# Kernel optimization log

Hardware: AMD Instinct MI355X
Metric: run time of the kernel (lower is better)

The kernel has to match this reference:

```python
import jax, jax.numpy as jnp
import numpy as np

N, D, R, O = 4096, 128, 256, 64


def setup_inputs() -> dict:
    key = jax.random.key(0)
    k1, k2, k3, k4 = jax.random.split(key, 4)
    X = jax.random.normal(k1, (N, D), dtype=jnp.float32)
    # Gaussian membership params per rule: centers and (positive) widths, shape [R, D]
    centers = 0.5 * jax.random.normal(k2, (R, D), dtype=jnp.float32)
    sigmas = 1.5 + jax.random.uniform(k3, (R, D), dtype=jnp.float32)  # in [1.5, 2.5]
    # Takagi-Sugeno per-rule linear coeffs [R, D+1, O] (last row = bias)
    coeffs = 0.02 * jax.random.normal(k4, (R, D + 1, O), dtype=jnp.float32)
    return {"X": X, "centers": centers, "sigmas": sigmas, "coeffs": coeffs}


def reference(X, centers, sigmas, coeffs):
    # Layer 1: Gaussian memberships for all rules at once: [N, R, D]
    diff = X[:, None, :] - centers[None, :, :]
    memb = jnp.exp(-(diff * diff) / (2.0 * sigmas * sigmas)[None, :, :])
    # Layer 2: rule strengths via product over input dims ('prod' strategy): [N, R]
    strengths = jnp.prod(memb, axis=2)
    # Layer 3: normalize across rules
    norm = strengths / (jnp.sum(strengths, axis=1, keepdims=True) + 1e-8)
    # Layer 4: per-rule linear consequents: [N, R, O]
    weighted = jnp.einsum('ni,rij->nrj', X, coeffs[:, :-1, :]) + coeffs[:, -1, :][None, :, :]
    # Layer 5: weighted combine over rules: [N, O]
    out = jnp.einsum('nr,nrj->nj', norm, weighted)
    # task='classification' -> Softmax(dim=1)
    return jax.nn.softmax(out, axis=1)
```

## Files before the change

kernel.cpp:

```cpp
#include <hip/hip_runtime.h>

#define N_SAMPLES 4096
#define D_IN      128
#define R_RULES   256
#define O_OUT     64
#define KPAD      136
#define NCHUNK    17
#define CH_I      8
#define NGROUPS   8

typedef _Float16 f16;
typedef _Float16 f16x2 __attribute__((ext_vector_type(2)));
typedef _Float16 f16x4 __attribute__((ext_vector_type(4)));
typedef _Float16 f16x8 __attribute__((ext_vector_type(8)));
typedef float    f32x4 __attribute__((ext_vector_type(4)));

__global__ __launch_bounds__(256) void anfis_prep_all(
    const float* __restrict__ coeffs, const float* __restrict__ centers,
    const float* __restrict__ sigmas, f16* __restrict__ Cp,
    f16* __restrict__ Bext) {
  __shared__ alignas(16) f16 T[64 * 32];
  __shared__ float red[4];
  const int bid = blockIdx.x;
  const int tid = threadIdx.x;

  if (bid < 1088) {
    const int g = bid / 136;
    const int i = bid - g * 136;
    const int rg = tid & 31;
    const int jb = tid >> 5;
    if (i < 129) {
      const float* src = coeffs + ((size_t)(g * 32 + rg) * 129 + i) * 64 + jb * 8;
      float4 a = reinterpret_cast<const float4*>(src)[0];
      float4 b = reinterpret_cast<const float4*>(src)[1];
      T[(jb * 8 + 0) * 32 + rg] = (f16)a.x;
      T[(jb * 8 + 1) * 32 + rg] = (f16)a.y;
      T[(jb * 8 + 2) * 32 + rg] = (f16)a.z;
      T[(jb * 8 + 3) * 32 + rg] = (f16)a.w;
      T[(jb * 8 + 4) * 32 + rg] = (f16)b.x;
      T[(jb * 8 + 5) * 32 + rg] = (f16)b.y;
      T[(jb * 8 + 6) * 32 + rg] = (f16)b.z;
      T[(jb * 8 + 7) * 32 + rg] = (f16)b.w;
    } else {
#pragma unroll
      for (int q = 0; q < 8; ++q) T[(jb * 8 + q) * 32 + rg] = (f16)0.0f;
    }
    __syncthreads();
    f16x8* dst = reinterpret_cast<f16x8*>(Cp + ((size_t)g * KPAD + i) * 2048);
    const int j = tid >> 2, blk = tid & 3;
    dst[(j << 2) | blk] = reinterpret_cast<const f16x8*>(T)[tid];
  } else {
    const int sub = tid >> 7;
    const int d = tid & 127;
    const int r = ((bid - 1088) << 1) + sub;
    const float c = centers[(size_t)r * 128 + d];
    const float s = sigmas[(size_t)r * 128 + d];
    const float iv = 0.5f / (s * s);
    const float b1 = -iv;
    const float b2 = 2.0f * c * iv;
    f16 b1h = (f16)b1; f16 b1l = (f16)(b1 - (float)b1h);
    f16 b2h = (f16)b2; f16 b2l = (f16)(b2 - (float)b2h);
    auto put = [&](int k, f16 v) {
      Bext[((size_t)(k >> 3) * 256 + r) * 8 + (k & 7)] = v;
    };
    put(d, b1h);
    put(128 + d, b1l);
    put(256 + d, b1h);
    put(384 + d, b2h);
    put(512 + d, b2l);
    put(640 + d, b2h);
    float p = -c * c * iv;
#pragma unroll
    for (int off = 32; off; off >>= 1) p += __shfl_xor(p, off, 64);
    if ((tid & 63) == 0) red[tid >> 6] = p;
    __syncthreads();
    if (d < 30) put(770 + d, (f16)0.0f);
    if (d == 0) {
      float k2 = red[sub * 2] + red[sub * 2 + 1];
      f16 h = (f16)k2; f16 l = (f16)(k2 - (float)h);
      put(768, h);
      put(769, l);
    }
  }
}

__global__ __launch_bounds__(512) void anfis_s16n(
    const float* __restrict__ X, const f16* __restrict__ Bext,
    f16* __restrict__ P) {
  __shared__ alignas(16) f16 Xq[16 * 512];
  __shared__ float rowsum[16][8];
  const int tid = threadIdx.x;
  const int m0 = blockIdx.x * 16;
  const int w = tid >> 6, lane = tid & 63;
  const int lm = lane & 15, quad = lane >> 4;

  if (tid < 256) {
    int m = tid >> 4, oct = tid & 15;
    const float* src = X + (size_t)(m0 + m) * 128 + oct * 8;
    float4 a = reinterpret_cast<const float4*>(src)[0];
    float4 b = reinterpret_cast<const float4*>(src)[1];
    float xs[8] = {a.x, a.y, a.z, a.w, b.x, b.y, b.z, b.w};
    f16x8 vh, vl, v2h, v2l;
#pragma unroll
    for (int q = 0; q < 8; ++q) {
      float x = xs[q];
      f16 h = (f16)x;   f16 l = (f16)(x - (float)h);
      float x2 = x * x;
      f16 h2 = (f16)x2; f16 l2 = (f16)(x2 - (float)h2);
      vh[q] = h; vl[q] = l; v2h[q] = h2; v2l[q] = l2;
    }
    f16x8* row = reinterpret_cast<f16x8*>(&Xq[m * 512]);
    int sw = m & 7;
    row[(0 * 16 + oct) ^ sw] = v2h;
    row[(1 * 16 + oct) ^ sw] = v2l;
    row[(2 * 16 + oct) ^ sw] = vh;
    row[(3 * 16 + oct) ^ sw] = vl;
  }
  __syncthreads();

  f32x4 acc[2] = {};
  const f16x8* arow = reinterpret_cast<const f16x8*>(&Xq[lm * 512]);
  const int asw = lm & 7;
  const int col0 = w * 32 + lm;

#pragma unroll
  for (int t = 0; t < 24; ++t) {
    const int seg = t >> 2;
    const int plane = (seg < 2) ? 0 : (seg == 2) ? 1 : (seg < 5) ? 2 : 3;
    const int o = t * 4 + quad;
    f16x8 av = arow[(plane * 16 + (o & 15)) ^ asw];
    const f16* bp = Bext + ((size_t)o * 256 + col0) * 8;
    f16x8 b0 = *reinterpret_cast<const f16x8*>(bp);
    f16x8 b1 = *reinterpret_cast<const f16x8*>(bp + 16 * 8);
    acc[0] = __builtin_amdgcn_mfma_f32_16x16x32_f16(av, b0, acc[0], 0, 0, 0);
    acc[1] = __builtin_amdgcn_mfma_f32_16x16x32_f16(av, b1, acc[1], 0, 0, 0);
  }
  {
    f16x8 av = {};
    if (quad == 0) { av[0] = (f16)1.0f; av[1] = (f16)1.0f; }
    const int o = 96 + quad;
    const f16* bp = Bext + ((size_t)o * 256 + col0) * 8;
    f16x8 b0 = *reinterpret_cast<const f16x8*>(bp);
    f16x8 b1 = *reinterpret_cast<const f16x8*>(bp + 16 * 8);
    acc[0] = __builtin_amdgcn_mfma_f32_16x16x32_f16(av, b0, acc[0], 0, 0, 0);
    acc[1] = __builtin_amdgcn_mfma_f32_16x16x32_f16(av, b1, acc[1], 0, 0, 0);
  }

  float e[2][4];
#pragma unroll
  for (int nf = 0; nf < 2; ++nf)
#pragma unroll
    for (int q = 0; q < 4; ++q) e[nf][q] = __expf(acc[nf][q]);

  float rp[4];
#pragma unroll
  for (int q = 0; q < 4; ++q) {
    rp[q] = e[0][q] + e[1][q];
#pragma unroll
    for (int msk = 1; msk < 16; msk <<= 1) rp[q] += __shfl_xor(rp[q], msk, 64);
  }
  if (lm == 0)
#pragma unroll
    for (int q = 0; q < 4; ++q) rowsum[quad * 4 + q][w] = rp[q];
  __syncthreads();

#pragma unroll
  for (int q = 0; q < 4; ++q) {
    const int row = quad * 4 + q;
    float s8 = 0.f;
#pragma unroll
    for (int w2 = 0; w2 < 8; ++w2) s8 += rowsum[row][w2];
    const float inv = 1.0f / (s8 + 1e-8f);
#pragma unroll
    for (int nf = 0; nf < 2; ++nf)
      P[(size_t)(m0 + row) * R_RULES + w * 32 + nf * 16 + lm] =
          (f16)(e[nf][q] * inv);
  }
}

__global__ __launch_bounds__(512) void anfis_main16(
    const float* __restrict__ X, const f16* __restrict__ P,
    const f16* __restrict__ Cp, float* __restrict__ part) {
  __shared__ alignas(16) f16 Xs[128 * KPAD];
  const int tid = threadIdx.x;
  const int g = blockIdx.x & 7;
  const int m0 = (blockIdx.x >> 3) * 128;
  const int w = tid >> 6, lane = tid & 63;
  const int mg = w >> 2;
  const int wc = w & 3;
  const int lm = lane & 15, quad = lane >> 4;

#pragma unroll
  for (int it = 0; it < 8; ++it) {
    int fi = tid + (it << 9);
    int m = fi >> 5, k4 = (fi & 31) << 2;
    float4 v = reinterpret_cast<const float4*>(X)[(size_t)(m0 + m) * 32 + (fi & 31)];
    f16x4 h = {(f16)v.x, (f16)v.y, (f16)v.z, (f16)v.w};
    *reinterpret_cast<f16x4*>(&Xs[m * KPAD + k4]) = h;
  }
  if (tid < 128) {
    f16x8 bias = {};
    bias[0] = (f16)1.0f;
    *reinterpret_cast<f16x8*>(&Xs[tid * KPAD + 128]) = bias;
  }

  union F8 { f16x8 v; f16x2 h[4]; };
  F8 pf[4];
#pragma unroll
  for (int mf = 0; mf < 4; ++mf) {
    int row = m0 + mg * 64 + mf * 16 + lm;
    pf[mf].v = *reinterpret_cast<const f16x8*>(
        &P[(size_t)row * R_RULES + g * 32 + quad * 8]);
  }

  __syncthreads();

  f32x4 acc[4] = {};
  const char* bsrc = (const char*)Cp + (size_t)g * KPAD * 4096 +
                     ((wc * 16 + lm) << 6) + (quad << 4);

  for (int c = 0; c < NCHUNK; ++c) {
    f16x8 xv[4];
#pragma unroll
    for (int mf = 0; mf < 4; ++mf)
      xv[mf] = *reinterpret_cast<const f16x8*>(
          &Xs[(mg * 64 + mf * 16 + lm) * KPAD + c * 8]);
#pragma unroll
    for (int ii = 0; ii < CH_I; ++ii) {
      f16x8 b0 = *reinterpret_cast<const f16x8*>(
          bsrc + (size_t)(c * 8 + ii) * 4096);
#pragma unroll
      for (int mf = 0; mf < 4; ++mf) {
        f16 xvv = xv[mf][ii];
        f16x2 xd = {xvv, xvv};
        F8 a;
        a.h[0] = pf[mf].h[0] * xd;
        a.h[1] = pf[mf].h[1] * xd;
        a.h[2] = pf[mf].h[2] * xd;
        a.h[3] = pf[mf].h[3] * xd;
        acc[mf] = __builtin_amdgcn_mfma_f32_16x16x32_f16(a.v, b0, acc[mf], 0, 0, 0);
      }
    }
  }

#pragma unroll
  for (int mf = 0; mf < 4; ++mf)
#pragma unroll
    for (int q = 0; q < 4; ++q) {
      int row = m0 + mg * 64 + mf * 16 + quad * 4 + q;
      int col = wc * 16 + lm;
      part[((size_t)g * N_SAMPLES + row) * O_OUT + col] = acc[mf][q];
    }
}

__global__ __launch_bounds__(256) void anfis_out(
    const float* __restrict__ part, float* __restrict__ out) {
  const int n = blockIdx.x * 4 + (threadIdx.x >> 6);
  const int lane = threadIdx.x & 63;
  const size_t stride = (size_t)N_SAMPLES * O_OUT;
  const float* p0 = part + (size_t)n * O_OUT + lane;
  float v = 0.f;
#pragma unroll
  for (int gg = 0; gg < 8; ++gg) v += p0[gg * stride];
  float mx = v;
#pragma unroll
  for (int off = 32; off; off >>= 1) mx = fmaxf(mx, __shfl_xor(mx, off, 64));
  float e = __expf(v - mx);
  float s = e;
#pragma unroll
  for (int off = 32; off; off >>= 1) s += __shfl_xor(s, off, 64);
  out[(size_t)n * O_OUT + lane] = e / s;
}

extern "C" void kernel_launch(void* const* d_in, const int* in_sizes, int n_in,
                              void* d_out, int out_size, void* d_ws, size_t ws_size,
                              hipStream_t stream) {
  const float* X       = (const float*)d_in[0];
  const float* centers = (const float*)d_in[1];
  const float* sigmas  = (const float*)d_in[2];
  const float* coeffs  = (const float*)d_in[3];
  float* out = (float*)d_out;

  float* part = (float*)d_ws;
  f16*   Cp   = (f16*)(part + (size_t)NGROUPS * N_SAMPLES * O_OUT);
  f16*   Bext = Cp + (size_t)NGROUPS * KPAD * 2048;
  f16*   P    = Bext + (size_t)100 * 256 * 8;

  anfis_prep_all<<<1088 + 128, 256, 0, stream>>>(coeffs, centers, sigmas, Cp, Bext);
  anfis_s16n<<<N_SAMPLES / 16, 512, 0, stream>>>(X, Bext, P);
  anfis_main16<<<256, 512, 0, stream>>>(X, P, Cp, part);
  anfis_out<<<N_SAMPLES / 4, 256, 0, stream>>>(part, out);
}
```

Baseline: 110.3 us.

## Rework consequent GEMM to 32x32 MFMA with LDS-staged double-buffered coefficients

The main consequent kernel now splits rules into 16 groups of 16 instead of 8 groups of 32 and uses 32x32x16 MFMA tiles. Coefficient tiles are streamed into shared memory with global_load_lds in a double-buffered loop, and X rows are read directly from global memory, replacing the shared-memory X staging. The prep kernel writes coefficients in a new layout to match, and the output kernel sums 16 partials instead of 8. The doubled partial buffer adds extra write and read traffic.

```diff
diff --git a/kernel.cpp b/kernel.cpp
--- a/kernel.cpp
+++ b/kernel.cpp
@@ -5,19 +5,19 @@
 #define R_RULES   256
 #define O_OUT     64
 #define KPAD      136
-#define NCHUNK    17
-#define CH_I      8
-#define NGROUPS   8
+#define NG16      16
+#define CP3_I     144
 
 typedef _Float16 f16;
 typedef _Float16 f16x2 __attribute__((ext_vector_type(2)));
 typedef _Float16 f16x4 __attribute__((ext_vector_type(4)));
 typedef _Float16 f16x8 __attribute__((ext_vector_type(8)));
 typedef float    f32x4 __attribute__((ext_vector_type(4)));
+typedef float    f32x16 __attribute__((ext_vector_type(16)));
 
 __global__ __launch_bounds__(256) void anfis_prep_all(
     const float* __restrict__ coeffs, const float* __restrict__ centers,
-    const float* __restrict__ sigmas, f16* __restrict__ Cp,
+    const float* __restrict__ sigmas, f16* __restrict__ Cp3,
     f16* __restrict__ Bext) {
   __shared__ alignas(16) f16 T[64 * 32];
   __shared__ float red[4];
@@ -25,12 +25,12 @@
   const int tid = threadIdx.x;
 
   if (bid < 1088) {
-    const int g = bid / 136;
-    const int i = bid - g * 136;
+    const int g8 = bid / 136;
+    const int i = bid - g8 * 136;
     const int rg = tid & 31;
     const int jb = tid >> 5;
     if (i < 129) {
-      const float* src = coeffs + ((size_t)(g * 32 + rg) * 129 + i) * 64 + jb * 8;
+      const float* src = coeffs + ((size_t)(g8 * 32 + rg) * 129 + i) * 64 + jb * 8;
       float4 a = reinterpret_cast<const float4*>(src)[0];
       float4 b = reinterpret_cast<const float4*>(src)[1];
       T[(jb * 8 + 0) * 32 + rg] = (f16)a.x;
@@ -46,9 +46,12 @@
       for (int q = 0; q < 8; ++q) T[(jb * 8 + q) * 32 + rg] = (f16)0.0f;
     }
     __syncthreads();
-    f16x8* dst = reinterpret_cast<f16x8*>(Cp + ((size_t)g * KPAD + i) * 2048);
-    const int j = tid >> 2, blk = tid & 3;
-    dst[(j << 2) | blk] = reinterpret_cast<const f16x8*>(T)[tid];
+    const int j = tid >> 2, oc = tid & 3;
+    const int g16 = g8 * 2 + (oc >> 1), rh = oc & 1;
+    const int jh = j >> 5, jl = j & 31;
+    f16x8* dst3 = reinterpret_cast<f16x8*>(Cp3);
+    dst3[(((size_t)g16 * CP3_I + i) * 2 + jh) * 64 + rh * 32 + jl] =
+        *reinterpret_cast<const f16x8*>(&T[j * 32 + oc * 8]);
   } else {
     const int sub = tid >> 7;
     const int d = tid & 127;
@@ -178,79 +181,104 @@
   }
 }
 
-__global__ __launch_bounds__(512) void anfis_main16(
+__global__ __launch_bounds__(512, 4) void anfis_rules32(
     const float* __restrict__ X, const f16* __restrict__ P,
-    const f16* __restrict__ Cp, float* __restrict__ part) {
-  __shared__ alignas(16) f16 Xs[128 * KPAD];
+    const f16* __restrict__ Cp3, float* __restrict__ part) {
+  __shared__ alignas(16) f16 Bs[2 * 16384];
   const int tid = threadIdx.x;
-  const int g = blockIdx.x & 7;
-  const int m0 = (blockIdx.x >> 3) * 128;
+  const int g = blockIdx.x & 15;
+  const int m0 = (blockIdx.x >> 4) * 128;
   const int w = tid >> 6, lane = tid & 63;
-  const int mg = w >> 2;
-  const int wc = w & 3;
-  const int lm = lane & 15, quad = lane >> 4;
-
-#pragma unroll
-  for (int it = 0; it < 8; ++it) {
-    int fi = tid + (it << 9);
-    int m = fi >> 5, k4 = (fi & 31) << 2;
-    float4 v = reinterpret_cast<const float4*>(X)[(size_t)(m0 + m) * 32 + (fi & 31)];
-    f16x4 h = {(f16)v.x, (f16)v.y, (f16)v.z, (f16)v.w};
-    *reinterpret_cast<f16x4*>(&Xs[m * KPAD + k4]) = h;
-  }
-  if (tid < 128) {
-    f16x8 bias = {};
-    bias[0] = (f16)1.0f;
-    *reinterpret_cast<f16x8*>(&Xs[tid * KPAD + 128]) = bias;
-  }
+  const int ms = w >> 1, jh = w & 1;
+  const int jl = lane & 31, rh = lane >> 5;
+  const int arow = m0 + ms * 32 + jl;
 
   union F8 { f16x8 v; f16x2 h[4]; };
-  F8 pf[4];
-#pragma unroll
-  for (int mf = 0; mf < 4; ++mf) {
-    int row = m0 + mg * 64 + mf * 16 + lm;
-    pf[mf].v = *reinterpret_cast<const f16x8*>(
-        &P[(size_t)row * R_RULES + g * 32 + quad * 8]);
-  }
-
+  F8 pf;
+  pf.v = *reinterpret_cast<const f16x8*>(&P[(size_t)arow * R_RULES + g * 16 + rh * 8]);
+
+  const float4* Xrow = reinterpret_cast<const float4*>(X + (size_t)arow * D_IN);
+  const char* cg = (const char*)Cp3 + (size_t)g * (CP3_I * 2048);
+  const int rdoff = jh * 512 + rh * 256 + jl * 8;
+
+  auto stage = [&](int buf, int ch) {
+    const char* gsrc = cg + (size_t)ch * 32768;
+#pragma unroll
+    for (int r = 0; r < 4; ++r) {
+      int off = (r << 13) + (w << 10);
+      __builtin_amdgcn_global_load_lds(
+          (const __attribute__((address_space(1))) unsigned int*)(gsrc + off + lane * 16),
+          (__attribute__((address_space(3))) unsigned int*)((char*)Bs + buf * 32768 + off),
+          16, 0, 0);
+    }
+  };
+
+  f16x8 xb[2][2];
+  auto cvt16 = [](float4 a, float4 b) {
+    f16x8 r = {(f16)a.x, (f16)a.y, (f16)a.z, (f16)a.w,
+               (f16)b.x, (f16)b.y, (f16)b.z, (f16)b.w};
+    return r;
+  };
+
+  stage(0, 0);
+  {
+    float4 f0 = Xrow[0], f1 = Xrow[1], f2 = Xrow[2], f3 = Xrow[3];
+    xb[0][0] = cvt16(f0, f1);
+    xb[0][1] = cvt16(f2, f3);
+  }
   __syncthreads();
 
-  f32x4 acc[4] = {};
-  const char* bsrc = (const char*)Cp + (size_t)g * KPAD * 4096 +
-                     ((wc * 16 + lm) << 6) + (quad << 4);
-
-  for (int c = 0; c < NCHUNK; ++c) {
-    f16x8 xv[4];
-#pragma unroll
-    for (int mf = 0; mf < 4; ++mf)
-      xv[mf] = *reinterpret_cast<const f16x8*>(
-          &Xs[(mg * 64 + mf * 16 + lm) * KPAD + c * 8]);
-#pragma unroll
-    for (int ii = 0; ii < CH_I; ++ii) {
-      f16x8 b0 = *reinterpret_cast<const f16x8*>(
-          bsrc + (size_t)(c * 8 + ii) * 4096);
-#pragma unroll
-      for (int mf = 0; mf < 4; ++mf) {
-        f16 xvv = xv[mf][ii];
-        f16x2 xd = {xvv, xvv};
-        F8 a;
-        a.h[0] = pf[mf].h[0] * xd;
-        a.h[1] = pf[mf].h[1] * xd;
-        a.h[2] = pf[mf].h[2] * xd;
-        a.h[3] = pf[mf].h[3] * xd;
-        acc[mf] = __builtin_amdgcn_mfma_f32_16x16x32_f16(a.v, b0, acc[mf], 0, 0, 0);
+  f32x16 acc = {};
+#pragma unroll
+  for (int ch = 0; ch < 8; ++ch) {
+    float4 f0, f1, f2, f3;
+    if (ch < 7) {
+      stage((ch + 1) & 1, ch + 1);
+      f0 = Xrow[(ch + 1) * 4 + 0];
+      f1 = Xrow[(ch + 1) * 4 + 1];
+      f2 = Xrow[(ch + 1) * 4 + 2];
+      f3 = Xrow[(ch + 1) * 4 + 3];
+    } else {
+      if (tid < 128) {
+        const char* gsrc = cg + (size_t)8 * 32768;
+        int off = (tid >> 6) << 10;
+        __builtin_amdgcn_global_load_lds(
+            (const __attribute__((address_space(1))) unsigned int*)(gsrc + off + lane * 16),
+            (__attribute__((address_space(3))) unsigned int*)((char*)Bs + off),
+            16, 0, 0);
       }
     }
-  }
-
-#pragma unroll
-  for (int mf = 0; mf < 4; ++mf)
-#pragma unroll
-    for (int q = 0; q < 4; ++q) {
-      int row = m0 + mg * 64 + mf * 16 + quad * 4 + q;
-      int col = wc * 16 + lm;
-      part[((size_t)g * N_SAMPLES + row) * O_OUT + col] = acc[mf][q];
-    }
+    const f16* bb = Bs + (ch & 1) * 16384;
+#pragma unroll
+    for (int t = 0; t < 16; ++t) {
+      f16 xs = xb[ch & 1][t >> 3][t & 7];
+      f16x2 xd = {xs, xs};
+      F8 a;
+      a.h[0] = pf.h[0] * xd;
+      a.h[1] = pf.h[1] * xd;
+      a.h[2] = pf.h[2] * xd;
+      a.h[3] = pf.h[3] * xd;
+      f16x8 b = *reinterpret_cast<const f16x8*>(bb + t * 1024 + rdoff);
+      acc = __builtin_amdgcn_mfma_f32_32x32x16_f16(a.v, b, acc, 0, 0, 0);
+    }
+    if (ch < 7) {
+      xb[(ch + 1) & 1][0] = cvt16(f0, f1);
+      xb[(ch + 1) & 1][1] = cvt16(f2, f3);
+    }
+    __syncthreads();
+  }
+
+  {
+    f16x8 b = *reinterpret_cast<const f16x8*>(Bs + rdoff);
+    acc = __builtin_amdgcn_mfma_f32_32x32x16_f16(pf.v, b, acc, 0, 0, 0);
+  }
+
+#pragma unroll
+  for (int q = 0; q < 16; ++q) {
+    int r = (q & 3) + 8 * (q >> 2) + 4 * rh;
+    part[((size_t)g * N_SAMPLES + (m0 + ms * 32 + r)) * O_OUT + jh * 32 + jl] =
+        acc[q];
+  }
 }
 
 __global__ __launch_bounds__(256) void anfis_out(
@@ -261,7 +289,7 @@
   const float* p0 = part + (size_t)n * O_OUT + lane;
   float v = 0.f;
 #pragma unroll
-  for (int gg = 0; gg < 8; ++gg) v += p0[gg * stride];
+  for (int gg = 0; gg < 16; ++gg) v += p0[gg * stride];
   float mx = v;
 #pragma unroll
   for (int off = 32; off; off >>= 1) mx = fmaxf(mx, __shfl_xor(mx, off, 64));
@@ -282,12 +310,12 @@
   float* out = (float*)d_out;
 
   float* part = (float*)d_ws;
-  f16*   Cp   = (f16*)(part + (size_t)NGROUPS * N_SAMPLES * O_OUT);
-  f16*   Bext = Cp + (size_t)NGROUPS * KPAD * 2048;
+  f16*   Cp3  = (f16*)(part + (size_t)NG16 * N_SAMPLES * O_OUT);
+  f16*   Bext = Cp3 + (size_t)NG16 * CP3_I * 1024;
   f16*   P    = Bext + (size_t)100 * 256 * 8;
 
-  anfis_prep_all<<<1088 + 128, 256, 0, stream>>>(coeffs, centers, sigmas, Cp, Bext);
+  anfis_prep_all<<<1088 + 128, 256, 0, stream>>>(coeffs, centers, sigmas, Cp3, Bext);
   anfis_s16n<<<N_SAMPLES / 16, 512, 0, stream>>>(X, Bext, P);
-  anfis_main16<<<256, 512, 0, stream>>>(X, P, Cp, part);
+  anfis_rules32<<<512, 512, 0, stream>>>(X, P, Cp3, part);
   anfis_out<<<N_SAMPLES / 4, 256, 0, stream>>>(part, out);
 }
```

After: 106.9 us. -3.1%, faster.
